# Performance work log

Measured on AMD Instinct MI355X. Metric: run time of the kernel, lower is better.

Reference implementation:

```python
import math
import jax, jax.numpy as jnp
import numpy as np

B, S, D, P, H = 8, 512, 1024, 128, 8  # batch, seq_len, dim, phase_dim, num_heads


def _layernorm(v, g, b, eps=1e-5):
    m = jnp.mean(v, axis=-1, keepdims=True)
    var = jnp.mean((v - m) ** 2, axis=-1, keepdims=True)
    return (v - m) * jax.lax.rsqrt(var + eps) * g + b


def setup_inputs() -> dict:
    key = jax.random.key(0)
    ks = jax.random.split(key, 12)
    s = 0.02
    f32 = jnp.float32
    return {
        'x':   jax.random.normal(ks[0], (B, S, D), f32),
        'Wa':  jax.random.normal(ks[1], (D, P), f32) * s,
        'ba':  jnp.zeros((P,), f32),
        'Wp':  jax.random.normal(ks[2], (D, P), f32) * s,
        'bp':  jnp.zeros((P,), f32),
        'g1':  jnp.ones((P,), f32),
        'bt1': jnp.zeros((P,), f32),
        'W1':  jax.random.normal(ks[3], (H, P, 2 * P), f32) * s,
        'bh1': jnp.zeros((H, 2 * P), f32),
        'W2':  jax.random.normal(ks[4], (H, 2 * P, P), f32) * s,
        'bh2': jnp.zeros((H, P), f32),
        'g2':  jnp.ones((P,), f32),
        'bt2': jnp.zeros((P,), f32),
        'Wo':  jax.random.normal(ks[5], (H * P, D), f32) * s,
        'bo':  jnp.zeros((D,), f32),
    }


def reference(x, Wa, ba, Wp, bp, g1, bt1, W1, bh1, W2, bh2, g2, bt2, Wo, bo):
    # amplitude/phase encoding; only the real part is ever used downstream
    amp = jnp.tanh(x @ Wa + ba)                       # [B,S,P]
    ph = jax.nn.sigmoid(x @ Wp + bp) * (2.0 * math.pi)
    real = amp * jnp.cos(ph)                          # [B,S,P]

    xn = _layernorm(real, g1, bt1)                    # shared norm1
    # per-head MLP, vectorized over heads via einsum
    t = jax.nn.gelu(jnp.einsum('bsp,hpq->hbsq', xn, W1) + bh1[:, None, None, :],
                    approximate=False)
    t = jnp.einsum('hbsq,hqp->hbsp', t, W2) + bh2[:, None, None, :]  # [H,B,S,P]

    # per-(head,sample,channel) self cross-correlation of the transformed
    # signal with itself (the conv1d(x, x, groups=batch) trick), padding=S//2,
    # truncated to S lags so it gates elementwise.
    C = H * B * P
    Tc = jnp.transpose(t, (0, 1, 3, 2)).reshape(1, C, S)   # [1, C, S]
    w = Tc.reshape(C, 1, S)                                 # one kernel per channel
    pad = S // 2
    inter = jax.lax.conv_general_dilated(Tc, w, (1,), [(pad, pad)],
                                         feature_group_count=C)  # [1, C, S+1]
    inter = inter[0, :, :S].reshape(H, B, P, S)
    inter = jnp.transpose(inter, (0, 1, 3, 2))              # [H,B,S,P]

    gated = real[None] * jax.nn.sigmoid(inter)              # [H,B,S,P]
    comb = jnp.transpose(gated, (1, 2, 0, 3))               # [B,S,H,P]
    nrm = _layernorm(comb, g2, bt2).reshape(B, S, H * P)    # norm2 per head
    return nrm @ Wo + bo + x
```

## Files before the change

### kernel.cpp

```cpp
#include <hip/hip_runtime.h>
#include <math.h>

typedef __attribute__((ext_vector_type(8))) short bf16x8_t;
typedef __attribute__((ext_vector_type(4))) float f32x4_t;

__device__ __forceinline__ float sigmoidf_(float x){ return 1.f/(1.f+expf(-x)); }
__device__ __forceinline__ float geluf_(float x){ return 0.5f*x*(1.f+erff(x*0.70710678118654752f)); }
__device__ __forceinline__ unsigned short f2bf(float x){
  unsigned int u = __float_as_uint(x);
  return (unsigned short)((u + 0x7fffu + ((u>>16)&1u)) >> 16);
}
__device__ __forceinline__ float bf2f(unsigned short h){
  return __uint_as_float(((unsigned int)h)<<16);
}
__device__ __forceinline__ bf16x8_t ldfrag(const unsigned short* p){
  union { bf16x8_t v; uint2 q[2]; } u;
  u.q[0] = *(const uint2*)p; u.q[1] = *(const uint2*)(p+4); return u.v;
}

__global__ __launch_bounds__(256) void bias_pack(const float* __restrict__ ba,
    const float* __restrict__ bp, float* __restrict__ bcat){
  int t = threadIdx.x; bcat[t] = (t<128)? ba[t] : bp[t-128];
}

__global__ __launch_bounds__(256) void transpose_split(
    const float* __restrict__ src, unsigned short* __restrict__ dhi,
    unsigned short* __restrict__ dlo, int R, int C)
{
  long zoff = (long)blockIdx.z * R * C;
  src += zoff; dhi += zoff; dlo += zoff;
  __shared__ float tile[32][33];
  int c0 = blockIdx.x*32, r0 = blockIdx.y*32;
  int j = threadIdx.x & 31, i0 = threadIdx.x >> 5;
  #pragma unroll
  for (int ii=0; ii<4; ++ii){ int i = i0 + ii*8;
    tile[i][j] = src[(long)(r0+i)*C + c0 + j]; }
  __syncthreads();
  #pragma unroll
  for (int ii=0; ii<4; ++ii){ int i = i0 + ii*8;
    float v = tile[j][i];
    unsigned short h = f2bf(v);
    dhi[(long)(c0+i)*R + r0 + j] = h;
    dlo[(long)(c0+i)*R + r0 + j] = f2bf(v - bf2f(h));
  }
}

template<int EPI>
__global__ __launch_bounds__(256) void gemm_mfma(
    const float* __restrict__ A, const unsigned short* __restrict__ Bhi,
    const unsigned short* __restrict__ Blo,
    const float* __restrict__ bias, const float* __restrict__ resid,
    float* __restrict__ C, int M, int N, int K,
    long sA, long sB, long sBias, long sC)
{
  int z = blockIdx.z;
  A += z*sA; Bhi += z*sB; Blo += z*sB; bias += z*sBias; C += z*sC;
  __shared__ unsigned short As_hi[64][68], As_lo[64][68];
  __shared__ unsigned short Bs_hi[128][68], Bs_lo[128][68];
  const int tid = threadIdx.x;
  const int lane = tid & 63, wv = tid >> 6;
  const int wr = wv >> 1, wc = wv & 1;
  const int mw = wr*32, nw = wc*64;
  const int la = lane & 15, kg = (lane >> 4) << 3;
  const int m0 = blockIdx.x * 64, n0 = blockIdx.y * 128;

  f32x4_t acc[2][4];
  #pragma unroll
  for (int i=0;i<2;++i)
    #pragma unroll
    for (int j=0;j<4;++j) acc[i][j] = (f32x4_t){0.f,0.f,0.f,0.f};

  for (int k0 = 0; k0 < K; k0 += 64) {
    float4 av[4]; uint4 bh4[4], bl4[4];
    #pragma unroll
    for (int r=0;r<4;++r){
      int ia = tid + r*256;
      av[r] = *(const float4*)(A + (long)(m0 + (ia>>4))*K + k0 + ((ia&15)<<2));
      int ib = tid + r*256;
      long bo = (long)(n0 + (ib>>3))*K + k0 + ((ib&7)<<3);
      bh4[r] = *(const uint4*)(Bhi + bo);
      bl4[r] = *(const uint4*)(Blo + bo);
    }
    __syncthreads();
    #pragma unroll
    for (int r=0;r<4;++r){
      int ia = tid + r*256;
      int arow = ia>>4, akc = (ia&15)<<2;
      float4 v = av[r];
      unsigned short h0=f2bf(v.x),h1=f2bf(v.y),h2=f2bf(v.z),h3=f2bf(v.w);
      uint2 whi; whi.x = (unsigned)h0 | ((unsigned)h1<<16); whi.y = (unsigned)h2 | ((unsigned)h3<<16);
      *(uint2*)&As_hi[arow][akc] = whi;
      unsigned short l0=f2bf(v.x-bf2f(h0)),l1=f2bf(v.y-bf2f(h1)),
                     l2=f2bf(v.z-bf2f(h2)),l3=f2bf(v.w-bf2f(h3));
      uint2 wlo; wlo.x = (unsigned)l0 | ((unsigned)l1<<16); wlo.y = (unsigned)l2 | ((unsigned)l3<<16);
      *(uint2*)&As_lo[arow][akc] = wlo;
      int ib = tid + r*256;
      int bn = ib>>3, bkc = (ib&7)<<3;
      uint2 t0; t0.x = bh4[r].x; t0.y = bh4[r].y;
      uint2 t1; t1.x = bh4[r].z; t1.y = bh4[r].w;
      *(uint2*)&Bs_hi[bn][bkc]   = t0;
      *(uint2*)&Bs_hi[bn][bkc+4] = t1;
      uint2 t2; t2.x = bl4[r].x; t2.y = bl4[r].y;
      uint2 t3; t3.x = bl4[r].z; t3.y = bl4[r].w;
      *(uint2*)&Bs_lo[bn][bkc]   = t2;
      *(uint2*)&Bs_lo[bn][bkc+4] = t3;
    }
    __syncthreads();
    #pragma unroll
    for (int kk=0; kk<2; ++kk){
      bf16x8_t ah[2], al[2], bh[4], bl[4];
      #pragma unroll
      for (int mf=0; mf<2; ++mf){
        ah[mf] = ldfrag(&As_hi[mw + mf*16 + la][kk*32 + kg]);
        al[mf] = ldfrag(&As_lo[mw + mf*16 + la][kk*32 + kg]);
      }
      #pragma unroll
      for (int nf=0; nf<4; ++nf){
        bh[nf] = ldfrag(&Bs_hi[nw + nf*16 + la][kk*32 + kg]);
        bl[nf] = ldfrag(&Bs_lo[nw + nf*16 + la][kk*32 + kg]);
      }
      #pragma unroll
      for (int mf=0; mf<2; ++mf)
        #pragma unroll
        for (int nf=0; nf<4; ++nf){
          acc[mf][nf] = __builtin_amdgcn_mfma_f32_16x16x32_bf16(ah[mf], bh[nf], acc[mf][nf], 0,0,0);
          acc[mf][nf] = __builtin_amdgcn_mfma_f32_16x16x32_bf16(ah[mf], bl[nf], acc[mf][nf], 0,0,0);
          acc[mf][nf] = __builtin_amdgcn_mfma_f32_16x16x32_bf16(al[mf], bh[nf], acc[mf][nf], 0,0,0);
        }
    }
  }
  #pragma unroll
  for (int mf=0; mf<2; ++mf){
    int grow0 = m0 + mw + mf*16 + ((lane>>4)<<2);
    #pragma unroll
    for (int nf=0; nf<4; ++nf){
      int gcol = n0 + nw + nf*16 + la;
      float bsv = bias[gcol];
      #pragma unroll
      for (int r=0;r<4;++r){
        int grow = grow0 + r;
        float v = acc[mf][nf][r] + bsv;
        if (EPI==1) v = geluf_(v);
        if (EPI==2) v += resid[(long)grow*N + gcol];
        C[(long)grow*N + gcol] = v;
      }
    }
  }
}

__global__ __launch_bounds__(256) void encode_ln_kernel(
    const float* __restrict__ E, const float* __restrict__ g1, const float* __restrict__ bt1,
    float* __restrict__ realp, float* __restrict__ xnp)
{
  int wv = threadIdx.x >> 6, lane = threadIdx.x & 63;
  long row = (long)blockIdx.x*4 + wv;
  const float* e = E + row*256;
  int p = lane*2;
  float2 a = *(const float2*)(e + p);
  float2 f = *(const float2*)(e + 128 + p);
  const float TWO_PI = 6.28318530717958647692f;
  float r0 = tanhf(a.x) * cosf(TWO_PI * sigmoidf_(f.x));
  float r1 = tanhf(a.y) * cosf(TWO_PI * sigmoidf_(f.y));
  float s = r0+r1, ss = r0*r0 + r1*r1;
  #pragma unroll
  for (int m=1;m<64;m<<=1){ s += __shfl_xor(s,m,64); ss += __shfl_xor(ss,m,64); }
  float mean = s * (1.f/128.f);
  float var  = ss * (1.f/128.f) - mean*mean;
  float inv  = rsqrtf(var + 1e-5f);
  float x0 = (r0-mean)*inv*g1[p]   + bt1[p];
  float x1 = (r1-mean)*inv*g1[p+1] + bt1[p+1];
  *(float2*)(realp + row*128 + p) = make_float2(r0,r1);
  *(float2*)(xnp   + row*128 + p) = make_float2(x0,x1);
}

__global__ __launch_bounds__(256) void autocorr_kernel(
    const float* __restrict__ t, float* __restrict__ sig)
{
  __shared__ float vp[4][1280];
  int bidx = blockIdx.x;
  int p4 = bidx & 31; int hb = bidx >> 5; int b = hb & 7, h = hb >> 3;
  float* vflat = &vp[0][0];
  for (int i = threadIdx.x; i < 4*1280; i += 256) vflat[i] = 0.f;
  __syncthreads();
  const float* tp = t + ((long)(h*4096 + b*512))*128 + p4*4;
  for (int idx = threadIdx.x; idx < 2048; idx += 256) {
    int s = idx >> 2, c = idx & 3;
    int li = 256 + s;
    vp[c][li + ((li>>3)<<1)] = tp[(long)s*128 + c];
  }
  __syncthreads();
  int wv = threadIdx.x >> 6, lane = threadIdx.x & 63;
  const float* V = vp[wv];
  int s0 = lane*8;
  float acc[8] = {0,0,0,0,0,0,0,0};
  float w[8], ba_[8];
  #pragma unroll
  for (int u=0;u<8;u+=2){ int li=s0+u; *(float2*)&w[u] = *(const float2*)&V[li + ((li>>3)<<1)]; }
  for (int kb=0; kb<512; kb+=8) {
    float nw[8];
    int nb0 = kb+8+s0;
    #pragma unroll
    for (int u=0;u<8;u+=2){ int li = nb0+u; *(float2*)&nw[u] = *(const float2*)&V[li + ((li>>3)<<1)]; }
    int lb0 = kb+256;
    #pragma unroll
    for (int u=0;u<8;u+=2){ int li = lb0+u; *(float2*)&ba_[u] = *(const float2*)&V[li + ((li>>3)<<1)]; }
    #pragma unroll
    for (int u=0;u<8;++u){
      float aa = ba_[u];
      #pragma unroll
      for (int j=0;j<8;++j){
        float wlj = (u+j<8) ? w[u+j] : nw[u+j-8];
        acc[j] = fmaf(aa, wlj, acc[j]);
      }
    }
    #pragma unroll
    for (int u=0;u<8;++u) w[u]=nw[u];
  }
  float* sp = sig + ((long)(h*4096 + b*512) + s0)*128 + p4*4 + wv;
  #pragma unroll
  for (int j=0;j<8;++j) sp[(long)j*128] = sigmoidf_(acc[j]);
}

__global__ __launch_bounds__(256) void gate_ln_kernel(
    const float* __restrict__ realp, const float* __restrict__ sig,
    const float* __restrict__ g2, const float* __restrict__ bt2,
    float* __restrict__ y)
{
  int wv = threadIdx.x >> 6, lane = threadIdx.x & 63;
  long r = (long)blockIdx.x*4 + wv;
  int h = (int)(r >> 12);
  long rem = r & 4095;
  int p = lane*2;
  float2 rv = *(const float2*)(realp + rem*128 + p);
  float2 sv = *(const float2*)(sig + r*128 + p);
  float a0 = rv.x*sv.x, a1 = rv.y*sv.y;
  float s = a0+a1, ss = a0*a0+a1*a1;
  #pragma unroll
  for (int m=1;m<64;m<<=1){ s += __shfl_xor(s,m,64); ss += __shfl_xor(ss,m,64); }
  float mean = s*(1.f/128.f);
  float var  = ss*(1.f/128.f) - mean*mean;
  float inv  = rsqrtf(var+1e-5f);
  float y0 = (a0-mean)*inv*g2[p]   + bt2[p];
  float y1 = (a1-mean)*inv*g2[p+1] + bt2[p+1];
  *(float2*)(y + rem*1024 + h*128 + p) = make_float2(y0,y1);
}

extern "C" void kernel_launch(void* const* d_in, const int* in_sizes, int n_in,
                              void* d_out, int out_size, void* d_ws, size_t ws_size,
                              hipStream_t stream)
{
  const float* x   = (const float*)d_in[0];
  const float* Wa  = (const float*)d_in[1];
  const float* ba  = (const float*)d_in[2];
  const float* Wp  = (const float*)d_in[3];
  const float* bp  = (const float*)d_in[4];
  const float* g1  = (const float*)d_in[5];
  const float* bt1 = (const float*)d_in[6];
  const float* W1  = (const float*)d_in[7];
  const float* bh1 = (const float*)d_in[8];
  const float* W2  = (const float*)d_in[9];
  const float* bh2 = (const float*)d_in[10];
  const float* g2  = (const float*)d_in[11];
  const float* bt2 = (const float*)d_in[12];
  const float* Wo  = (const float*)d_in[13];
  const float* bo  = (const float*)d_in[14];

  char* p = (char*)d_ws;
  auto alloc = [&](size_t bytes)->char*{ char* r = p; p += (bytes + 255) & ~(size_t)255; return r; };
  float* bcat = (float*)alloc(256*4);
  unsigned short* WcatT_hi = (unsigned short*)alloc(256*1024*2);
  unsigned short* WcatT_lo = (unsigned short*)alloc(256*1024*2);
  unsigned short* W1T_hi   = (unsigned short*)alloc(8*256*128*2);
  unsigned short* W1T_lo   = (unsigned short*)alloc(8*256*128*2);
  unsigned short* W2T_hi   = (unsigned short*)alloc(8*128*256*2);
  unsigned short* W2T_lo   = (unsigned short*)alloc(8*128*256*2);
  unsigned short* WoT_hi   = (unsigned short*)alloc(1024*1024*2);
  unsigned short* WoT_lo   = (unsigned short*)alloc(1024*1024*2);
  float* E     = (float*)alloc((size_t)4096*256*4);
  float* realp = (float*)alloc((size_t)4096*128*4);
  float* xnp   = (float*)alloc((size_t)4096*128*4);
  float* hid   = (float*)alloc((size_t)8*4096*256*4);
  float* tbuf  = (float*)alloc((size_t)8*4096*128*4);
  float* sigb  = hid;
  float* ybuf  = tbuf;
  float* out   = (float*)d_out;

  bias_pack<<<1,256,0,stream>>>(ba,bp,bcat);
  transpose_split<<<dim3(4,32,1),256,0,stream>>>(Wa, WcatT_hi, WcatT_lo, 1024,128);
  transpose_split<<<dim3(4,32,1),256,0,stream>>>(Wp, WcatT_hi+131072, WcatT_lo+131072, 1024,128);
  transpose_split<<<dim3(8,4,8),256,0,stream>>>(W1, W1T_hi, W1T_lo, 128,256);
  transpose_split<<<dim3(4,8,8),256,0,stream>>>(W2, W2T_hi, W2T_lo, 256,128);
  transpose_split<<<dim3(32,32,1),256,0,stream>>>(Wo, WoT_hi, WoT_lo, 1024,1024);

  gemm_mfma<0><<<dim3(64,2,1),256,0,stream>>>(x, WcatT_hi, WcatT_lo, bcat, nullptr, E,
                                              4096,256,1024, 0,0,0,0);
  encode_ln_kernel<<<1024,256,0,stream>>>(E,g1,bt1,realp,xnp);
  gemm_mfma<1><<<dim3(64,2,8),256,0,stream>>>(xnp, W1T_hi, W1T_lo, bh1, nullptr, hid,
                                              4096,256,128, 0, (long)256*128, 256, (long)4096*256);
  gemm_mfma<0><<<dim3(64,1,8),256,0,stream>>>(hid, W2T_hi, W2T_lo, bh2, nullptr, tbuf,
                                              4096,128,256, (long)4096*256, (long)128*256, 128, (long)4096*128);
  autocorr_kernel<<<2048,256,0,stream>>>(tbuf, sigb);
  gate_ln_kernel<<<8192,256,0,stream>>>(realp, sigb, g2, bt2, ybuf);
  gemm_mfma<2><<<dim3(64,8,1),256,0,stream>>>(ybuf, WoT_hi, WoT_lo, bo, x, out,
                                              4096,1024,1024, 0,0,0,0);
}
```

Baseline: 288.4 us.

## Store intermediates as pre-split bf16 and halve autocorrelation work via symmetry

Intermediate activations (normalized input, hidden MLP output, transformed signal, sigmoid gate, norm2 output) are now written as bf16 hi/lo pairs, or as single bf16, in place of fp32. A new GEMM variant reads these pre-split operands directly with 16-byte loads instead of splitting fp32 on the fly. The autocorrelation kernel uses the symmetry of the self-correlation to compute only non-negative lags plus the lag-256 term, then mirrors results, which roughly halves its FMAs and shrinks shared memory. The signal and gate are kept in single bf16, which costs some accuracy.

```diff
diff --git a/kernel.cpp b/kernel.cpp
--- a/kernel.cpp
+++ b/kernel.cpp
@@ -16,6 +16,9 @@
 __device__ __forceinline__ bf16x8_t ldfrag(const unsigned short* p){
   union { bf16x8_t v; uint2 q[2]; } u;
   u.q[0] = *(const uint2*)p; u.q[1] = *(const uint2*)(p+4); return u.v;
+}
+__device__ __forceinline__ bf16x8_t ldfrag16(const unsigned short* p){
+  union { bf16x8_t v; uint4 q; } u; u.q = *(const uint4*)p; return u.v;
 }
 
 __global__ __launch_bounds__(256) void bias_pack(const float* __restrict__ ba,
@@ -148,9 +151,118 @@
   }
 }
 
+template<int EPI>
+__global__ __launch_bounds__(256) void gemm_mfma_s(
+    const unsigned short* __restrict__ Ahi, const unsigned short* __restrict__ Alo,
+    const unsigned short* __restrict__ Bhi, const unsigned short* __restrict__ Blo,
+    const float* __restrict__ bias, const float* __restrict__ resid,
+    float* __restrict__ Cf, unsigned short* __restrict__ Chi, unsigned short* __restrict__ Clo,
+    int M, int N, int K, long sA, long sB, long sBias, long sC)
+{
+  int z = blockIdx.z;
+  Ahi += (long)z*sA; Alo += (long)z*sA; Bhi += (long)z*sB; Blo += (long)z*sB;
+  bias += (long)z*sBias;
+  const long co = (long)z*sC;
+  __shared__ unsigned short As_hi[64][72], As_lo[64][72];
+  __shared__ unsigned short Bs_hi[128][72], Bs_lo[128][72];
+  const int tid = threadIdx.x;
+  const int lane = tid & 63, wv = tid >> 6;
+  const int wr = wv >> 1, wc = wv & 1;
+  const int mw = wr*32, nw = wc*64;
+  const int la = lane & 15, kg = (lane >> 4) << 3;
+  const int m0 = blockIdx.x * 64, n0 = blockIdx.y * 128;
+
+  f32x4_t acc[2][4];
+  #pragma unroll
+  for (int i=0;i<2;++i)
+    #pragma unroll
+    for (int j=0;j<4;++j) acc[i][j] = (f32x4_t){0.f,0.f,0.f,0.f};
+
+  for (int k0 = 0; k0 < K; k0 += 64) {
+    uint4 ah4[2], al4[2], bh4[4], bl4[4];
+    #pragma unroll
+    for (int r=0;r<2;++r){
+      int id = tid + r*256;
+      long off = (long)(m0 + (id>>3))*K + k0 + ((id&7)<<3);
+      ah4[r] = *(const uint4*)(Ahi + off);
+      al4[r] = *(const uint4*)(Alo + off);
+    }
+    #pragma unroll
+    for (int r=0;r<4;++r){
+      int id = tid + r*256;
+      long off = (long)(n0 + (id>>3))*K + k0 + ((id&7)<<3);
+      bh4[r] = *(const uint4*)(Bhi + off);
+      bl4[r] = *(const uint4*)(Blo + off);
+    }
+    __syncthreads();
+    #pragma unroll
+    for (int r=0;r<2;++r){
+      int id = tid + r*256;
+      int row = id>>3, c = (id&7)<<3;
+      *(uint4*)&As_hi[row][c] = ah4[r];
+      *(uint4*)&As_lo[row][c] = al4[r];
+    }
+    #pragma unroll
+    for (int r=0;r<4;++r){
+      int id = tid + r*256;
+      int row = id>>3, c = (id&7)<<3;
+      *(uint4*)&Bs_hi[row][c] = bh4[r];
+      *(uint4*)&Bs_lo[row][c] = bl4[r];
+    }
+    __syncthreads();
+    #pragma unroll
+    for (int kk=0; kk<2; ++kk){
+      bf16x8_t ah[2], al[2], bh[4], bl[4];
+      #pragma unroll
+      for (int mf=0; mf<2; ++mf){
+        ah[mf] = ldfrag16(&As_hi[mw + mf*16 + la][kk*32 + kg]);
+        al[mf] = ldfrag16(&As_lo[mw + mf*16 + la][kk*32 + kg]);
+      }
+      #pragma unroll
+      for (int nf=0; nf<4; ++nf){
+        bh[nf] = ldfrag16(&Bs_hi[nw + nf*16 + la][kk*32 + kg]);
+        bl[nf] = ldfrag16(&Bs_lo[nw + nf*16 + la][kk*32 + kg]);
+      }
+      #pragma unroll
+      for (int mf=0; mf<2; ++mf)
+        #pragma unroll
+        for (int nf=0; nf<4; ++nf){
+          acc[mf][nf] = __builtin_amdgcn_mfma_f32_16x16x32_bf16(ah[mf], bh[nf], acc[mf][nf], 0,0,0);
+          acc[mf][nf] = __builtin_amdgcn_mfma_f32_16x16x32_bf16(ah[mf], bl[nf], acc[mf][nf], 0,0,0);
+          acc[mf][nf] = __builtin_amdgcn_mfma_f32_16x16x32_bf16(al[mf], bh[nf], acc[mf][nf], 0,0,0);
+        }
+    }
+  }
+  #pragma unroll
+  for (int mf=0; mf<2; ++mf){
+    int grow0 = m0 + mw + mf*16 + ((lane>>4)<<2);
+    #pragma unroll
+    for (int nf=0; nf<4; ++nf){
+      int gcol = n0 + nw + nf*16 + la;
+      float bsv = bias[gcol];
+      #pragma unroll
+      for (int r=0;r<4;++r){
+        int grow = grow0 + r;
+        float v = acc[mf][nf][r] + bsv;
+        long idx = co + (long)grow*N + gcol;
+        if (EPI==1){
+          float g = geluf_(v);
+          unsigned short h = f2bf(g);
+          Chi[idx] = h;
+          Clo[idx] = f2bf(g - bf2f(h));
+        } else if (EPI==3){
+          Chi[idx] = f2bf(v);
+        } else {
+          Cf[(long)grow*N + gcol] = v + resid[(long)grow*N + gcol];
+        }
+      }
+    }
+  }
+}
+
 __global__ __launch_bounds__(256) void encode_ln_kernel(
     const float* __restrict__ E, const float* __restrict__ g1, const float* __restrict__ bt1,
-    float* __restrict__ realp, float* __restrict__ xnp)
+    float* __restrict__ realp, unsigned short* __restrict__ xnh, unsigned short* __restrict__ xnl)
 {
   int wv = threadIdx.x >> 6, lane = threadIdx.x & 63;
   long row = (long)blockIdx.x*4 + wv;
@@ -170,61 +282,75 @@
   float x0 = (r0-mean)*inv*g1[p]   + bt1[p];
   float x1 = (r1-mean)*inv*g1[p+1] + bt1[p+1];
   *(float2*)(realp + row*128 + p) = make_float2(r0,r1);
-  *(float2*)(xnp   + row*128 + p) = make_float2(x0,x1);
+  unsigned short h0 = f2bf(x0), h1 = f2bf(x1);
+  *(unsigned int*)(xnh + row*128 + p) = (unsigned)h0 | ((unsigned)h1<<16);
+  unsigned short l0 = f2bf(x0 - bf2f(h0)), l1 = f2bf(x1 - bf2f(h1));
+  *(unsigned int*)(xnl + row*128 + p) = (unsigned)l0 | ((unsigned)l1<<16);
 }
 
 __global__ __launch_bounds__(256) void autocorr_kernel(
-    const float* __restrict__ t, float* __restrict__ sig)
-{
-  __shared__ float vp[4][1280];
+    const unsigned short* __restrict__ tb, unsigned short* __restrict__ sig)
+{
+  __shared__ float vp[4][968];
   int bidx = blockIdx.x;
   int p4 = bidx & 31; int hb = bidx >> 5; int b = hb & 7, h = hb >> 3;
   float* vflat = &vp[0][0];
-  for (int i = threadIdx.x; i < 4*1280; i += 256) vflat[i] = 0.f;
+  for (int i = threadIdx.x; i < 4*968; i += 256) vflat[i] = 0.f;
   __syncthreads();
-  const float* tp = t + ((long)(h*4096 + b*512))*128 + p4*4;
+  const unsigned short* tp = tb + ((long)(h*4096 + b*512))*128 + p4*4;
   for (int idx = threadIdx.x; idx < 2048; idx += 256) {
     int s = idx >> 2, c = idx & 3;
-    int li = 256 + s;
-    vp[c][li + ((li>>3)<<1)] = tp[(long)s*128 + c];
+    vp[c][s + ((s>>3)<<1)] = bf2f(tp[(long)s*128 + c]);
   }
   __syncthreads();
   int wv = threadIdx.x >> 6, lane = threadIdx.x & 63;
   const float* V = vp[wv];
-  int s0 = lane*8;
-  float acc[8] = {0,0,0,0,0,0,0,0};
-  float w[8], ba_[8];
-  #pragma unroll
-  for (int u=0;u<8;u+=2){ int li=s0+u; *(float2*)&w[u] = *(const float2*)&V[li + ((li>>3)<<1)]; }
-  for (int kb=0; kb<512; kb+=8) {
-    float nw[8];
-    int nb0 = kb+8+s0;
-    #pragma unroll
-    for (int u=0;u<8;u+=2){ int li = nb0+u; *(float2*)&nw[u] = *(const float2*)&V[li + ((li>>3)<<1)]; }
-    int lb0 = kb+256;
-    #pragma unroll
-    for (int u=0;u<8;u+=2){ int li = lb0+u; *(float2*)&ba_[u] = *(const float2*)&V[li + ((li>>3)<<1)]; }
+  int lb = lane*4;
+  float acc[4] = {0,0,0,0};
+  float cur[8], nxt[8], aa[8];
+  #pragma unroll
+  for (int u=0;u<8;u+=2){ int li = lb+u; *(float2*)&cur[u] = *(const float2*)&V[li + ((li>>3)<<1)]; }
+  for (int t0=0; t0<512; t0+=8){
+    #pragma unroll
+    for (int u=0;u<8;u+=2){ int li = t0+8+lb+u; *(float2*)&nxt[u] = *(const float2*)&V[li + ((li>>3)<<1)]; }
+    #pragma unroll
+    for (int u=0;u<8;u+=2){ int li = t0+u; *(float2*)&aa[u] = *(const float2*)&V[li + ((li>>3)<<1)]; }
     #pragma unroll
     for (int u=0;u<8;++u){
-      float aa = ba_[u];
-      #pragma unroll
-      for (int j=0;j<8;++j){
-        float wlj = (u+j<8) ? w[u+j] : nw[u+j-8];
-        acc[j] = fmaf(aa, wlj, acc[j]);
-      }
-    }
-    #pragma unroll
-    for (int u=0;u<8;++u) w[u]=nw[u];
-  }
-  float* sp = sig + ((long)(h*4096 + b*512) + s0)*128 + p4*4 + wv;
-  #pragma unroll
-  for (int j=0;j<8;++j) sp[(long)j*128] = sigmoidf_(acc[j]);
+      float a = aa[u];
+      #pragma unroll
+      for (int j=0;j<4;++j){
+        int w = u+j;
+        float wl = (w<8)? cur[w] : nxt[w-8];
+        acc[j] = fmaf(a, wl, acc[j]);
+      }
+    }
+    #pragma unroll
+    for (int u=0;u<8;++u) cur[u]=nxt[u];
+  }
+  float r256 = 0.f;
+  #pragma unroll
+  for (int u=0;u<4;++u){
+    int t = lb + u; int t2 = t + 256;
+    r256 = fmaf(V[t + ((t>>3)<<1)], V[t2 + ((t2>>3)<<1)], r256);
+  }
+  #pragma unroll
+  for (int m=1;m<64;m<<=1) r256 += __shfl_xor(r256, m, 64);
+  unsigned short* sp = sig + ((long)(h*4096 + b*512))*128 + p4*4 + wv;
+  #pragma unroll
+  for (int j=0;j<4;++j){
+    int lam = lb + j;
+    unsigned short bv = f2bf(sigmoidf_(acc[j]));
+    sp[(long)(256+lam)*128] = bv;
+    if (lam > 0) sp[(long)(256-lam)*128] = bv;
+  }
+  if (lane == 0) sp[0] = f2bf(sigmoidf_(r256));
 }
 
 __global__ __launch_bounds__(256) void gate_ln_kernel(
-    const float* __restrict__ realp, const float* __restrict__ sig,
+    const float* __restrict__ realp, const unsigned short* __restrict__ sig,
     const float* __restrict__ g2, const float* __restrict__ bt2,
-    float* __restrict__ y)
+    unsigned short* __restrict__ yh, unsigned short* __restrict__ yl)
 {
   int wv = threadIdx.x >> 6, lane = threadIdx.x & 63;
   long r = (long)blockIdx.x*4 + wv;
@@ -232,8 +358,10 @@
   long rem = r & 4095;
   int p = lane*2;
   float2 rv = *(const float2*)(realp + rem*128 + p);
-  float2 sv = *(const float2*)(sig + r*128 + p);
-  float a0 = rv.x*sv.x, a1 = rv.y*sv.y;
+  unsigned int sv2 = *(const unsigned int*)(sig + r*128 + p);
+  float s0 = bf2f((unsigned short)(sv2 & 0xffffu));
+  float s1 = bf2f((unsigned short)(sv2 >> 16));
+  float a0 = rv.x*s0, a1 = rv.y*s1;
   float s = a0+a1, ss = a0*a0+a1*a1;
   #pragma unroll
   for (int m=1;m<64;m<<=1){ s += __shfl_xor(s,m,64); ss += __shfl_xor(ss,m,64); }
@@ -242,7 +370,11 @@
   float inv  = rsqrtf(var+1e-5f);
   float y0 = (a0-mean)*inv*g2[p]   + bt2[p];
   float y1 = (a1-mean)*inv*g2[p+1] + bt2[p+1];
-  *(float2*)(y + rem*1024 + h*128 + p) = make_float2(y0,y1);
+  long o = rem*1024 + h*128 + p;
+  unsigned short h0 = f2bf(y0), h1 = f2bf(y1);
+  *(unsigned int*)(yh + o) = (unsigned)h0 | ((unsigned)h1<<16);
+  unsigned short l0 = f2bf(y0 - bf2f(h0)), l1 = f2bf(y1 - bf2f(h1));
+  *(unsigned int*)(yl + o) = (unsigned)l0 | ((unsigned)l1<<16);
 }
 
 extern "C" void kernel_launch(void* const* d_in, const int* in_sizes, int n_in,
@@ -278,11 +410,14 @@
   unsigned short* WoT_lo   = (unsigned short*)alloc(1024*1024*2);
   float* E     = (float*)alloc((size_t)4096*256*4);
   float* realp = (float*)alloc((size_t)4096*128*4);
-  float* xnp   = (float*)alloc((size_t)4096*128*4);
-  float* hid   = (float*)alloc((size_t)8*4096*256*4);
-  float* tbuf  = (float*)alloc((size_t)8*4096*128*4);
-  float* sigb  = hid;
-  float* ybuf  = tbuf;
+  unsigned short* xnh = (unsigned short*)alloc((size_t)4096*128*2);
+  unsigned short* xnl = (unsigned short*)alloc((size_t)4096*128*2);
+  unsigned short* hidh = (unsigned short*)alloc((size_t)8*4096*256*2);
+  unsigned short* hidl = (unsigned short*)alloc((size_t)8*4096*256*2);
+  unsigned short* tbuf = (unsigned short*)alloc((size_t)8*4096*128*2);
+  unsigned short* sigb = hidh;
+  unsigned short* yh   = tbuf;
+  unsigned short* yl   = hidl;
   float* out   = (float*)d_out;
 
   bias_pack<<<1,256,0,stream>>>(ba,bp,bcat);
@@ -294,13 +429,16 @@
 
   gemm_mfma<0><<<dim3(64,2,1),256,0,stream>>>(x, WcatT_hi, WcatT_lo, bcat, nullptr, E,
                                               4096,256,1024, 0,0,0,0);
-  encode_ln_kernel<<<1024,256,0,stream>>>(E,g1,bt1,realp,xnp);
-  gemm_mfma<1><<<dim3(64,2,8),256,0,stream>>>(xnp, W1T_hi, W1T_lo, bh1, nullptr, hid,
-                                              4096,256,128, 0, (long)256*128, 256, (long)4096*256);
-  gemm_mfma<0><<<dim3(64,1,8),256,0,stream>>>(hid, W2T_hi, W2T_lo, bh2, nullptr, tbuf,
-                                              4096,128,256, (long)4096*256, (long)128*256, 128, (long)4096*128);
+  encode_ln_kernel<<<1024,256,0,stream>>>(E,g1,bt1,realp,xnh,xnl);
+  gemm_mfma_s<1><<<dim3(64,2,8),256,0,stream>>>(xnh, xnl, W1T_hi, W1T_lo, bh1, nullptr,
+                                                nullptr, hidh, hidl,
+                                                4096,256,128, 0, (long)256*128, 256, (long)4096*256);
+  gemm_mfma_s<3><<<dim3(64,1,8),256,0,stream>>>(hidh, hidl, W2T_hi, W2T_lo, bh2, nullptr,
+                                                nullptr, tbuf, nullptr,
+                                                4096,128,256, (long)4096*256, (long)128*256, 128, (long)4096*128);
   autocorr_kernel<<<2048,256,0,stream>>>(tbuf, sigb);
-  gate_ln_kernel<<<8192,256,0,stream>>>(realp, sigb, g2, bt2, ybuf);
-  gemm_mfma<2><<<dim3(64,8,1),256,0,stream>>>(ybuf, WoT_hi, WoT_lo, bo, x, out,
-                                              4096,1024,1024, 0,0,0,0);
-}
+  gate_ln_kernel<<<8192,256,0,stream>>>(realp, sigb, g2, bt2, yh, yl);
+  gemm_mfma_s<2><<<dim3(64,8,1),256,0,stream>>>(yh, yl, WoT_hi, WoT_lo, bo, x,
+                                                out, nullptr, nullptr,
+                                                4096,1024,1024, 0,0,0,0);
+}
```

After: 357.8 us. +24.1%, slower.

## Exploit autocorrelation symmetry and store W2 output channel-major for autocorr

Applied to the files above, without the earlier changes.

The autocorrelation kernel now computes only the non-negative lags, half the previous count, and mirrors each result to its symmetric negative lag. Lag 256 gets its own wave-reduced dot product. This roughly halves the FMA work per channel. The W2 GEMM gets a new epilogue that writes its output transposed ([H,P,B*S]) with float4 stores, so autocorr loads contiguous rows instead of strided ones and needs less shared memory. The transposed GEMM stores are strided across lanes, which may cost some write efficiency.

```diff
diff --git a/kernel.cpp b/kernel.cpp
--- a/kernel.cpp
+++ b/kernel.cpp
@@ -54,7 +54,7 @@
     long sA, long sB, long sBias, long sC)
 {
   int z = blockIdx.z;
-  A += z*sA; Bhi += z*sB; Blo += z*sB; bias += z*sBias; C += z*sC;
+  A += (long)z*sA; Bhi += (long)z*sB; Blo += (long)z*sB; bias += (long)z*sBias; C += (long)z*sC;
   __shared__ unsigned short As_hi[64][68], As_lo[64][68];
   __shared__ unsigned short Bs_hi[128][68], Bs_lo[128][68];
   const int tid = threadIdx.x;
@@ -136,13 +136,20 @@
     for (int nf=0; nf<4; ++nf){
       int gcol = n0 + nw + nf*16 + la;
       float bsv = bias[gcol];
-      #pragma unroll
-      for (int r=0;r<4;++r){
-        int grow = grow0 + r;
-        float v = acc[mf][nf][r] + bsv;
-        if (EPI==1) v = geluf_(v);
-        if (EPI==2) v += resid[(long)grow*N + gcol];
-        C[(long)grow*N + gcol] = v;
+      if (EPI==4){
+        float4 o;
+        o.x = acc[mf][nf][0] + bsv; o.y = acc[mf][nf][1] + bsv;
+        o.z = acc[mf][nf][2] + bsv; o.w = acc[mf][nf][3] + bsv;
+        *(float4*)(C + (long)gcol*M + grow0) = o;
+      } else {
+        #pragma unroll
+        for (int r=0;r<4;++r){
+          int grow = grow0 + r;
+          float v = acc[mf][nf][r] + bsv;
+          if (EPI==1) v = geluf_(v);
+          if (EPI==2) v += resid[(long)grow*N + gcol];
+          C[(long)grow*N + gcol] = v;
+        }
       }
     }
   }
@@ -174,51 +181,62 @@
 }
 
 __global__ __launch_bounds__(256) void autocorr_kernel(
-    const float* __restrict__ t, float* __restrict__ sig)
-{
-  __shared__ float vp[4][1280];
+    const float* __restrict__ tT, float* __restrict__ sig)
+{
+  __shared__ float vp[4][968];
   int bidx = blockIdx.x;
   int p4 = bidx & 31; int hb = bidx >> 5; int b = hb & 7, h = hb >> 3;
   float* vflat = &vp[0][0];
-  for (int i = threadIdx.x; i < 4*1280; i += 256) vflat[i] = 0.f;
+  for (int i = threadIdx.x; i < 4*968; i += 256) vflat[i] = 0.f;
   __syncthreads();
-  const float* tp = t + ((long)(h*4096 + b*512))*128 + p4*4;
+  const float* tp = tT + ((long)(h*128 + p4*4))*4096 + b*512;
   for (int idx = threadIdx.x; idx < 2048; idx += 256) {
-    int s = idx >> 2, c = idx & 3;
-    int li = 256 + s;
-    vp[c][li + ((li>>3)<<1)] = tp[(long)s*128 + c];
+    int c = idx >> 9, s = idx & 511;
+    vp[c][s + ((s>>3)<<1)] = tp[(long)c*4096 + s];
   }
   __syncthreads();
   int wv = threadIdx.x >> 6, lane = threadIdx.x & 63;
   const float* V = vp[wv];
-  int s0 = lane*8;
-  float acc[8] = {0,0,0,0,0,0,0,0};
-  float w[8], ba_[8];
-  #pragma unroll
-  for (int u=0;u<8;u+=2){ int li=s0+u; *(float2*)&w[u] = *(const float2*)&V[li + ((li>>3)<<1)]; }
-  for (int kb=0; kb<512; kb+=8) {
-    float nw[8];
-    int nb0 = kb+8+s0;
-    #pragma unroll
-    for (int u=0;u<8;u+=2){ int li = nb0+u; *(float2*)&nw[u] = *(const float2*)&V[li + ((li>>3)<<1)]; }
-    int lb0 = kb+256;
-    #pragma unroll
-    for (int u=0;u<8;u+=2){ int li = lb0+u; *(float2*)&ba_[u] = *(const float2*)&V[li + ((li>>3)<<1)]; }
+  int lb = lane*4;
+  float acc[4] = {0,0,0,0};
+  float cur[8], nxt[8], aa[8];
+  #pragma unroll
+  for (int u=0;u<8;u+=2){ int li = lb+u; *(float2*)&cur[u] = *(const float2*)&V[li + ((li>>3)<<1)]; }
+  for (int t0=0; t0<512; t0+=8){
+    #pragma unroll
+    for (int u=0;u<8;u+=2){ int li = t0+8+lb+u; *(float2*)&nxt[u] = *(const float2*)&V[li + ((li>>3)<<1)]; }
+    #pragma unroll
+    for (int u=0;u<8;u+=2){ int li = t0+u; *(float2*)&aa[u] = *(const float2*)&V[li + ((li>>3)<<1)]; }
     #pragma unroll
     for (int u=0;u<8;++u){
-      float aa = ba_[u];
+      float a = aa[u];
       #pragma unroll
-      for (int j=0;j<8;++j){
-        float wlj = (u+j<8) ? w[u+j] : nw[u+j-8];
-        acc[j] = fmaf(aa, wlj, acc[j]);
+      for (int j=0;j<4;++j){
+        int w = u+j;
+        float wl = (w<8)? cur[w] : nxt[w-8];
+        acc[j] = fmaf(a, wl, acc[j]);
       }
     }
     #pragma unroll
-    for (int u=0;u<8;++u) w[u]=nw[u];
-  }
-  float* sp = sig + ((long)(h*4096 + b*512) + s0)*128 + p4*4 + wv;
-  #pragma unroll
-  for (int j=0;j<8;++j) sp[(long)j*128] = sigmoidf_(acc[j]);
+    for (int u=0;u<8;++u) cur[u]=nxt[u];
+  }
+  float r256 = 0.f;
+  #pragma unroll
+  for (int u=0;u<4;++u){
+    int t = lb + u; int t2 = t + 256;
+    r256 = fmaf(V[t + ((t>>3)<<1)], V[t2 + ((t2>>3)<<1)], r256);
+  }
+  #pragma unroll
+  for (int m=1;m<64;m<<=1) r256 += __shfl_xor(r256, m, 64);
+  float* sp = sig + ((long)(h*4096 + b*512))*128 + p4*4 + wv;
+  #pragma unroll
+  for (int j=0;j<4;++j){
+    int lam = lb + j;
+    float bv = sigmoidf_(acc[j]);
+    sp[(long)(256+lam)*128] = bv;
+    if (lam > 0) sp[(long)(256-lam)*128] = bv;
+  }
+  if (lane == 0) sp[0] = sigmoidf_(r256);
 }
 
 __global__ __launch_bounds__(256) void gate_ln_kernel(
@@ -280,7 +298,7 @@
   float* realp = (float*)alloc((size_t)4096*128*4);
   float* xnp   = (float*)alloc((size_t)4096*128*4);
   float* hid   = (float*)alloc((size_t)8*4096*256*4);
-  float* tbuf  = (float*)alloc((size_t)8*4096*128*4);
+  float* tbuf  = (float*)alloc((size_t)8*128*4096*4);
   float* sigb  = hid;
   float* ybuf  = tbuf;
   float* out   = (float*)d_out;
@@ -297,8 +315,8 @@
   encode_ln_kernel<<<1024,256,0,stream>>>(E,g1,bt1,realp,xnp);
   gemm_mfma<1><<<dim3(64,2,8),256,0,stream>>>(xnp, W1T_hi, W1T_lo, bh1, nullptr, hid,
                                               4096,256,128, 0, (long)256*128, 256, (long)4096*256);
-  gemm_mfma<0><<<dim3(64,1,8),256,0,stream>>>(hid, W2T_hi, W2T_lo, bh2, nullptr, tbuf,
-                                              4096,128,256, (long)4096*256, (long)128*256, 128, (long)4096*128);
+  gemm_mfma<4><<<dim3(64,1,8),256,0,stream>>>(hid, W2T_hi, W2T_lo, bh2, nullptr, tbuf,
+                                              4096,128,256, (long)4096*256, (long)128*256, 128, (long)128*4096);
   autocorr_kernel<<<2048,256,0,stream>>>(tbuf, sigb);
   gate_ln_kernel<<<8192,256,0,stream>>>(realp, sigb, g2, bt2, ybuf);
   gemm_mfma<2><<<dim3(64,8,1),256,0,stream>>>(ybuf, WoT_hi, WoT_lo, bo, x, out,
```

New measurement: 263.2 us. 8.7% less time.
